# Performance work log

Hardware: AMD Instinct MI355X
Metric: run time of the kernel (lower is better)

## Reference

```python
import jax, jax.numpy as jnp
import numpy as np

B, L, R, F = 16, 64, 256, 64
LIG_NIN, REC_NIN, EIN, EEMB = 32, 40, 16, 16
DEG = 8
E_LIG, E_REC = B * L * DEG, B * R * DEG
NL = 3
PNAMES = ["emb_nW", "emb_nb", "emb_eW", "emb_eb", "hidW", "hidb", "ln0_g", "ln0_b",
          "efW", "efb", "convb", "outW", "outb", "lng", "lnb"]
INT_NAMES = ("lig_src", "lig_dst", "rec_src", "rec_dst")


def _lrelu(v):
    return jax.nn.leaky_relu(v, 0.01)


def _ln(x, g, b):
    m = x.mean(-1, keepdims=True)
    v = ((x - m) ** 2).mean(-1, keepdims=True)
    return (x - m) / jnp.sqrt(v + 1e-5) * g + b


def _side(node_x, edge_x, src, dst, n_nodes, p):
    # GraphEmbedding: linear node/edge embedding
    eh = edge_x @ p["emb_eW"] + p["emb_eb"]                      # [E, EEMB]
    h = _lrelu(node_x @ p["emb_nW"] + p["emb_nb"]) @ p["hidW"] + p["hidb"]
    h = _ln(h, p["ln0_g"], p["ln0_b"])                           # [N, F]
    deg = jax.ops.segment_sum(jnp.ones(src.shape[0], jnp.float32), dst, num_segments=n_nodes)
    deg = jnp.maximum(deg, 1.0)[:, None]
    prev = []
    for i in range(NL):
        hh = _lrelu(h)
        # NNConv: per-edge F x F weight conditioned on edge features
        We = (eh @ p["efW"][i] + p["efb"][i]).reshape(-1, F, F)  # [E, F, F]
        msg = jnp.einsum('ei,eio->eo', hh[src], We)              # [E, F]
        agg = jax.ops.segment_sum(msg, dst, num_segments=n_nodes) / deg + p["convb"][i]
        h = _ln(_lrelu(agg) @ p["outW"][i] + p["outb"][i], p["lng"][i], p["lnb"][i])
        if i >= 2:  # residual to layer i-2
            h = h + prev[i - 2]
        prev.append(h)
    return h


def _forward(fl, lig_src, lig_dst, rec_src, rec_dst):
    lig_p = {n: fl["lig_" + n] for n in PNAMES}
    rec_p = {n: fl["rec_" + n] for n in PNAMES}
    lig_h = _side(fl["lig_x"], fl["lig_e"], lig_src, lig_dst, B * L, lig_p)
    rec_h = _side(fl["rec_x"], fl["rec_e"], rec_src, rec_dst, B * R, rec_p)
    # per-graph einsum('lf,rf->lr') scoring, batched since graphs are equal-sized
    op = jnp.einsum('blf,brf->blr', lig_h.reshape(B, L, F), rec_h.reshape(B, R, F))
    out = op.mean((1, 2))
    return out, op


def setup_inputs() -> dict:
    key = jax.random.key(0)
    it = iter(jax.random.split(key, 80))
    def nrm(shape, s=0.1):
        return jax.random.normal(next(it), shape, jnp.float32) * s
    inp = {}
    inp["lig_x"] = nrm((B * L, LIG_NIN), 1.0)
    inp["rec_x"] = nrm((B * R, REC_NIN), 1.0)
    inp["lig_e"] = nrm((E_LIG, EIN), 1.0)
    inp["rec_e"] = nrm((E_REC, EIN), 1.0)
    def edges(npg, epg, k1, k2):
        offs = (jnp.arange(B) * npg)[:, None]
        s = (jax.random.randint(k1, (B, epg), 0, npg) + offs).reshape(-1).astype(jnp.int32)
        d = (jax.random.randint(k2, (B, epg), 0, npg) + offs).reshape(-1).astype(jnp.int32)
        return s, d
    inp["lig_src"], inp["lig_dst"] = edges(L, L * DEG, next(it), next(it))
    inp["rec_src"], inp["rec_dst"] = edges(R, R * DEG, next(it), next(it))
    for pre, nin in (("lig", LIG_NIN), ("rec", REC_NIN)):
        inp[pre + "_emb_nW"] = nrm((nin, F)); inp[pre + "_emb_nb"] = nrm((F,))
        inp[pre + "_emb_eW"] = nrm((EIN, EEMB)); inp[pre + "_emb_eb"] = nrm((EEMB,))
        inp[pre + "_hidW"] = nrm((F, F)); inp[pre + "_hidb"] = nrm((F,))
        inp[pre + "_ln0_g"] = jnp.ones((F,)); inp[pre + "_ln0_b"] = jnp.zeros((F,))
        inp[pre + "_efW"] = nrm((NL, EEMB, F * F), 0.05); inp[pre + "_efb"] = nrm((NL, F * F), 0.05)
        inp[pre + "_convb"] = nrm((NL, F))
        inp[pre + "_outW"] = nrm((NL, F, F)); inp[pre + "_outb"] = nrm((NL, F))
        inp[pre + "_lng"] = jnp.ones((NL, F)); inp[pre + "_lnb"] = jnp.zeros((NL, F))
    return inp


def reference(lig_x, rec_x, lig_e, rec_e, lig_src, lig_dst, rec_src, rec_dst,
              lig_emb_nW, lig_emb_nb, lig_emb_eW, lig_emb_eb, lig_hidW, lig_hidb,
              lig_ln0_g, lig_ln0_b, lig_efW, lig_efb, lig_convb, lig_outW, lig_outb,
              lig_lng, lig_lnb,
              rec_emb_nW, rec_emb_nb, rec_emb_eW, rec_emb_eb, rec_hidW, rec_hidb,
              rec_ln0_g, rec_ln0_b, rec_efW, rec_efb, rec_convb, rec_outW, rec_outb,
              rec_lng, rec_lnb):
    all_args = dict(locals())
    fl = {k: v for k, v in all_args.items() if k not in INT_NAMES}
    return _forward(fl, lig_src, lig_dst, rec_src, rec_dst)
```

## Files before the change

### kernel.cpp

```cpp
#include <hip/hip_runtime.h>
#include <hip/hip_bf16.h>

#define NLIG 1024
#define NREC 4096
#define NTOT 5120
#define ELIG 8192
#define ETOT 40960
#define TPAD 1092

typedef __bf16 bf16x8 __attribute__((ext_vector_type(8)));
typedef float f32x4 __attribute__((ext_vector_type(4)));

struct Params {
  const float *lig_x, *rec_x, *lig_e, *rec_e;
  const int *lig_src, *lig_dst, *rec_src, *rec_dst;
  const float *nW[2], *nb[2], *eW[2], *eb[2], *hW[2], *hb[2], *g0[2], *b0[2];
  const float *efW[2], *efb[2], *convb[2], *outW[2], *outb[2], *lng[2], *lnb[2];
  float *aggA, *aggB, *prev0, *eh;
  __bf16 *Abf, *Wp;
  int *deg;
  float *out;
};

__device__ __forceinline__ float lrelu(float v){ return v > 0.f ? v : 0.01f * v; }

__device__ __forceinline__ float wsum(float v){
  #pragma unroll
  for (int off = 32; off > 0; off >>= 1) v += __shfl_xor(v, off, 64);
  return v;
}

__global__ __launch_bounds__(256) void k_pre(Params p){
  __shared__ float sW[2][256], sb[2][16], sx[4][40], st[4][64];
  const int tid = threadIdx.x, bid = blockIdx.x;
  const int lane = tid & 63, wid = tid >> 6;
  const int gtid = bid*256 + tid, gwave = bid*4 + wid;

  sW[0][tid] = p.eW[0][tid];
  sW[1][tid] = p.eW[1][tid];
  if (tid < 16){ sb[0][tid] = p.eb[0][tid]; sb[1][tid] = p.eb[1][tid]; }
  __syncthreads();

  if (gtid < 52224){
    int l  = gtid & 63;
    int t2 = gtid >> 6;
    int kk = t2 & 1;
    int t3 = t2 >> 1;
    int ct = t3 % 68;
    int sl = t3 / 68;
    int side = sl / 3, layer = sl % 3;
    int ocol = ct*16 + (l & 15);
    int kslot = ocol >> 6, oo = ocol & 63;
    const float* src = (kslot < 16)
        ? (p.efW[side] + (size_t)layer*16*4096 + (size_t)kslot*4096)
        : (p.efb[side] + (size_t)layer*4096);
    bf16x8 w;
    #pragma unroll
    for (int j = 0; j < 8; j++){
      int i = kk*32 + (l >> 4)*8 + j;
      w[j] = (__bf16)src[i*64 + oo];
    }
    ((bf16x8*)p.Wp)[(size_t)sl*68*2*64 + (ct*2 + kk)*64 + l] = w;
  }

  if (gtid < ETOT){
    int e = gtid;
    int side = e >= ELIG;
    int el = side ? e - ELIG : e;
    const float* ex = (side ? p.rec_e : p.lig_e) + (size_t)el * 16;
    float x[16];
    #pragma unroll
    for (int j = 0; j < 16; j += 4){
      float4 v = *(const float4*)(ex + j);
      x[j] = v.x; x[j+1] = v.y; x[j+2] = v.z; x[j+3] = v.w;
    }
    float s[16];
    #pragma unroll
    for (int k = 0; k < 16; k++){
      float acc = sb[side][k];
      #pragma unroll
      for (int j = 0; j < 16; j++) acc += x[j] * sW[side][j*16 + k];
      s[k] = acc;
    }
    float* ehp = p.eh + (size_t)e * 16;
    #pragma unroll
    for (int k = 0; k < 16; k += 4)
      *(float4*)(ehp + k) = make_float4(s[k], s[k+1], s[k+2], s[k+3]);
  }

  for (int i = gtid; i < NTOT*64; i += 65536){ p.aggA[i] = 0.f; p.aggB[i] = 0.f; }
  if (gtid < 16) p.out[gtid] = 0.f;

  for (int n = gwave; n < NTOT; n += 1024){
    int side = n >= NLIG;
    int nl = side ? n - NLIG : n;
    int nin = side ? 40 : 32;
    const float* x = (side ? p.rec_x : p.lig_x) + (size_t)nl * nin;
    if (lane < nin) sx[wid][lane] = x[lane];
    float tv = p.nb[side][lane];
    const float* nw = p.nW[side];
    for (int j = 0; j < nin; j++) tv += sx[wid][j] * nw[j*64 + lane];
    st[wid][lane] = lrelu(tv);
    float hv = p.hb[side][lane];
    const float* hw = p.hW[side];
    #pragma unroll 8
    for (int j = 0; j < 64; j++) hv += st[wid][j] * hw[j*64 + lane];
    float m = wsum(hv) * (1.f/64.f);
    float d = hv - m;
    float v = wsum(d*d) * (1.f/64.f);
    float o = d * rsqrtf(v + 1e-5f) * p.g0[side][lane] + p.b0[side][lane];
    p.Abf[(size_t)n*64 + lane] = (__bf16)lrelu(o);
  }
}

__global__ __launch_bounds__(1024) void k_layer(Params p, int layer){
  const int tid = threadIdx.x, bid = blockIdx.x;
  const int lane = tid & 63, wid = tid >> 6;
  int side, r0, gr0, ebase, ecnt, egbase;
  const int *srcArr, *dstArr;
  if (bid < 64){
    side = 0; int b = bid >> 2, w = bid & 3;
    r0 = b*64 + w*16; gr0 = r0; ebase = b*512; ecnt = 512; egbase = ebase;
    srcArr = p.lig_src; dstArr = p.lig_dst;
  } else {
    side = 1; int g = bid - 64; int b = g >> 4, w = g & 15;
    r0 = b*256 + w*16; gr0 = NLIG + r0; ebase = b*2048; ecnt = 2048; egbase = ELIG + ebase;
    srcArr = p.rec_src; dstArr = p.rec_dst;
  }
  float* aggR = (layer == 1) ? p.aggA : p.aggB;
  float* aggW = (layer == 1) ? p.aggB : p.aggA;

  __shared__ __bf16 Tl[16][TPAD];
  __shared__ __bf16 albf[16][64];
  __shared__ float sa[16][64];
  __shared__ unsigned int elist[2048];
  __shared__ int scnt[16], sbase[16], scur[16], dcnt[16];

  if (tid < 16){ scnt[tid] = 0; dcnt[tid] = 0; }
  __syncthreads();

  for (int i = tid; i < ecnt; i += 1024){
    int s = srcArr[ebase + i];
    if ((unsigned)(s - r0) < 16u) atomicAdd(&scnt[s - r0], 1);
    if (layer == 0){
      int d = dstArr[ebase + i];
      if ((unsigned)(d - r0) < 16u) atomicAdd(&dcnt[d - r0], 1);
    }
  }
  __syncthreads();
  if (tid < 64){
    int v = (lane < 16) ? scnt[lane] : 0;
    int pre = v;
    #pragma unroll
    for (int off = 1; off < 16; off <<= 1){
      int u = __shfl_up(pre, off, 64);
      if (lane >= off) pre += u;
    }
    if (lane < 16){ sbase[lane] = pre - v; scur[lane] = pre - v; }
  }
  if (layer == 0 && tid < 16) p.deg[gr0 + tid] = dcnt[tid];
  __syncthreads();
  for (int i = tid; i < ecnt; i += 1024){
    int s = srcArr[ebase + i];
    if ((unsigned)(s - r0) < 16u){
      int d = dstArr[ebase + i];
      int pos = atomicAdd(&scur[s - r0], 1);
      elist[pos] = ((unsigned)d << 16) | (unsigned)i;
    }
  }

  if (layer > 0){
    int lm1 = layer - 1;
    int rl = wid;
    int n = gr0 + rl;
    float a = aggR[(size_t)n*64 + lane];
    aggR[(size_t)n*64 + lane] = 0.f;
    float dg = fmaxf((float)p.deg[n], 1.f);
    a = lrelu(a / dg + p.convb[side][lm1*64 + lane]);
    sa[wid][lane] = a;
    float hv = p.outb[side][lm1*64 + lane];
    const float* ow = p.outW[side] + (size_t)lm1*4096;
    #pragma unroll 8
    for (int j = 0; j < 64; j++) hv += sa[wid][j] * ow[j*64 + lane];
    float m = wsum(hv) * (1.f/64.f);
    float d = hv - m;
    float v = wsum(d*d) * (1.f/64.f);
    float o = d * rsqrtf(v + 1e-5f) * p.lng[side][lm1*64 + lane] + p.lnb[side][lm1*64 + lane];
    if (layer == 1) p.prev0[(size_t)n*64 + lane] = o;
    albf[rl][lane] = (__bf16)lrelu(o);
  }
  __syncthreads();

  bf16x8 a0, a1;
  if (layer == 0){
    const bf16x8* A = (const bf16x8*)(p.Abf + (size_t)(gr0 + (lane & 15))*64 + (lane >> 4)*8);
    a0 = A[0]; a1 = A[4];
  } else {
    #pragma unroll
    for (int j = 0; j < 8; j++){
      a0[j] = albf[lane & 15][(lane >> 4)*8 + j];
      a1[j] = albf[lane & 15][32 + (lane >> 4)*8 + j];
    }
  }
  const bf16x8* Wb = (const bf16x8*)p.Wp + (size_t)(side*3 + layer)*68*2*64;
  int orow = (lane >> 4)*4, ocol = lane & 15;
  for (int ct = wid; ct < 68; ct += 16){
    bf16x8 b0 = Wb[(ct*2 + 0)*64 + lane];
    bf16x8 b1 = Wb[(ct*2 + 1)*64 + lane];
    f32x4 d = {0.f, 0.f, 0.f, 0.f};
    d = __builtin_amdgcn_mfma_f32_16x16x32_bf16(a0, b0, d, 0, 0, 0);
    d = __builtin_amdgcn_mfma_f32_16x16x32_bf16(a1, b1, d, 0, 0, 0);
    int col = ct*16 + ocol;
    Tl[orow+0][col] = (__bf16)d[0];
    Tl[orow+1][col] = (__bf16)d[1];
    Tl[orow+2][col] = (__bf16)d[2];
    Tl[orow+3][col] = (__bf16)d[3];
  }
  __syncthreads();

  {
    int s = wid;
    int cnt = scnt[s];
    if (cnt > 0){
      float t[17];
      #pragma unroll
      for (int k = 0; k < 17; k++) t[k] = (float)Tl[s][k*64 + lane];
      int base = sbase[s];
      auto doe = [&](int idx){
        unsigned v = elist[base + idx];
        int gd = (int)(v >> 16) + (side ? NLIG : 0);
        int leid = (int)(v & 0xffffu);
        const float4* ehp = (const float4*)(p.eh + (size_t)(egbase + leid)*16);
        float4 v0 = ehp[0], v1 = ehp[1], v2 = ehp[2], v3 = ehp[3];
        float m = t[16];
        m += v0.x*t[0]  + v0.y*t[1]  + v0.z*t[2]  + v0.w*t[3];
        m += v1.x*t[4]  + v1.y*t[5]  + v1.z*t[6]  + v1.w*t[7];
        m += v2.x*t[8]  + v2.y*t[9]  + v2.z*t[10] + v2.w*t[11];
        m += v3.x*t[12] + v3.y*t[13] + v3.z*t[14] + v3.w*t[15];
        atomicAdd(&aggW[(size_t)gd*64 + lane], m);
      };
      int i = 0;
      for (; i + 2 <= cnt; i += 2){ doe(i); doe(i+1); }
      if (i < cnt) doe(i);
    }
  }
}

__global__ __launch_bounds__(1024) void k_final(Params p){
  const int tid = threadIdx.x, bid = blockIdx.x;
  const int lane = tid & 63, wid = tid >> 6;
  int b = bid >> 4, rt = bid & 15;
  __shared__ float slh[64][65];
  __shared__ float srh[16][65];
  __shared__ float owl[2][4096];
  __shared__ float sa[16][64];
  __shared__ float ps[16];

  for (int idx = tid; idx < 4096; idx += 1024){
    owl[0][idx] = p.outW[0][2*4096 + idx];
    owl[1][idx] = p.outW[1][2*4096 + idx];
  }
  __syncthreads();

  for (int rr = wid; rr < 80; rr += 16){
    int side = rr >= 64;
    int n = side ? (NLIG + b*256 + rt*16 + (rr - 64)) : (b*64 + rr);
    float a = p.aggA[(size_t)n*64 + lane];
    float dg = fmaxf((float)p.deg[n], 1.f);
    a = lrelu(a / dg + p.convb[side][128 + lane]);
    sa[wid][lane] = a;
    float hv = p.outb[side][128 + lane];
    const float* ow = &owl[side][0];
    #pragma unroll 8
    for (int j = 0; j < 64; j++) hv += sa[wid][j] * ow[j*64 + lane];
    float m = wsum(hv) * (1.f/64.f);
    float d = hv - m;
    float v = wsum(d*d) * (1.f/64.f);
    float o = d * rsqrtf(v + 1e-5f) * p.lng[side][128 + lane] + p.lnb[side][128 + lane];
    o += p.prev0[(size_t)n*64 + lane];
    if (side) srh[rr - 64][lane] = o; else slh[rr][lane] = o;
  }
  __syncthreads();

  int r = tid & 15, lg = tid >> 4;
  float acc = 0.f;
  #pragma unroll 8
  for (int f = 0; f < 64; f++) acc += slh[lg][f] * srh[r][f];
  p.out[16 + (size_t)b*16384 + (size_t)lg*256 + rt*16 + r] = acc;

  float psum = wsum(acc);
  if (lane == 0) ps[wid] = psum;
  __syncthreads();
  if (tid == 0){
    float s = 0.f;
    #pragma unroll
    for (int i = 0; i < 16; i++) s += ps[i];
    atomicAdd(&p.out[b], s * (1.f/16384.f));
  }
}

extern "C" void kernel_launch(void* const* d_in, const int* in_sizes, int n_in,
                              void* d_out, int out_size, void* d_ws, size_t ws_size,
                              hipStream_t stream){
  Params p;
  p.lig_x  = (const float*)d_in[0];
  p.rec_x  = (const float*)d_in[1];
  p.lig_e  = (const float*)d_in[2];
  p.rec_e  = (const float*)d_in[3];
  p.lig_src = (const int*)d_in[4];
  p.lig_dst = (const int*)d_in[5];
  p.rec_src = (const int*)d_in[6];
  p.rec_dst = (const int*)d_in[7];
  for (int s = 0; s < 2; s++){
    const int o = 8 + s*15;
    p.nW[s]   = (const float*)d_in[o+0];  p.nb[s]   = (const float*)d_in[o+1];
    p.eW[s]   = (const float*)d_in[o+2];  p.eb[s]   = (const float*)d_in[o+3];
    p.hW[s]   = (const float*)d_in[o+4];  p.hb[s]   = (const float*)d_in[o+5];
    p.g0[s]   = (const float*)d_in[o+6];  p.b0[s]   = (const float*)d_in[o+7];
    p.efW[s]  = (const float*)d_in[o+8];  p.efb[s]  = (const float*)d_in[o+9];
    p.convb[s]= (const float*)d_in[o+10]; p.outW[s] = (const float*)d_in[o+11];
    p.outb[s] = (const float*)d_in[o+12]; p.lng[s]  = (const float*)d_in[o+13];
    p.lnb[s]  = (const float*)d_in[o+14];
  }
  char* W = (char*)d_ws;
  p.aggA  = (float*)W;  W += (size_t)NTOT*64*4;
  p.aggB  = (float*)W;  W += (size_t)NTOT*64*4;
  p.prev0 = (float*)W;  W += (size_t)NTOT*64*4;
  p.eh    = (float*)W;  W += (size_t)ETOT*16*4;
  p.Abf   = (__bf16*)W; W += (size_t)NTOT*64*2;
  p.Wp    = (__bf16*)W; W += (size_t)2*3*68*2*64*8*2;
  p.deg   = (int*)W;    W += (size_t)NTOT*4;
  p.out   = (float*)d_out;

  k_pre<<<256, 256, 0, stream>>>(p);
  k_layer<<<320, 1024, 0, stream>>>(p, 0);
  k_layer<<<320, 1024, 0, stream>>>(p, 1);
  k_layer<<<320, 1024, 0, stream>>>(p, 2);
  k_final<<<256, 1024, 0, stream>>>(p);
}
```

Before: 116.3 us.

## Build edge buckets once in pre-kernel and reuse across all layers

Moves the per-block edge bucketing (counting by source row, prefix scan, scatter into an edge list) out of each of the three layer launches and into the pre-kernel, which now runs on 320 blocks and writes the buckets, bases and counts to global workspace. Each layer kernel then reads its bucket list from global memory with a coalesced per-wave load and broadcasts entries by shuffle, instead of rebuilding the list in shared memory every launch. This removes repeated scans of the src/dst arrays, the shared atomics and two barriers per layer, and frees the 8 KB shared edge list. The cost is extra global traffic for the bucket arrays and more work in the pre-kernel. The layer kernel also gains a min-blocks hint in its launch bounds.

```diff
diff --git a/kernel.cpp b/kernel.cpp
--- a/kernel.cpp
+++ b/kernel.cpp
@@ -19,6 +19,8 @@
   float *aggA, *aggB, *prev0, *eh;
   __bf16 *Abf, *Wp;
   int *deg;
+  unsigned *bkt;
+  int *bktbase, *bktcnt;
   float *out;
 };
 
@@ -30,8 +32,24 @@
   return v;
 }
 
+__device__ __forceinline__ void window(int bid, int& side, int& r0, int& gr0,
+                                       int& ebase, int& ecnt, int& egbase,
+                                       const int*& srcArr, const int*& dstArr,
+                                       const Params& p){
+  if (bid < 64){
+    side = 0; int b = bid >> 2, w = bid & 3;
+    r0 = b*64 + w*16; gr0 = r0; ebase = b*512; ecnt = 512; egbase = ebase;
+    srcArr = p.lig_src; dstArr = p.lig_dst;
+  } else {
+    side = 1; int g = bid - 64; int b = g >> 4, w = g & 15;
+    r0 = b*256 + w*16; gr0 = NLIG + r0; ebase = b*2048; ecnt = 2048; egbase = ELIG + ebase;
+    srcArr = p.rec_src; dstArr = p.rec_dst;
+  }
+}
+
 __global__ __launch_bounds__(256) void k_pre(Params p){
   __shared__ float sW[2][256], sb[2][16], sx[4][40], st[4][64];
+  __shared__ int scnt[16], sbase[16], scur[16], dcnt[16];
   const int tid = threadIdx.x, bid = blockIdx.x;
   const int lane = tid & 63, wid = tid >> 6;
   const int gtid = bid*256 + tid, gwave = bid*4 + wid;
@@ -39,6 +57,7 @@
   sW[0][tid] = p.eW[0][tid];
   sW[1][tid] = p.eW[1][tid];
   if (tid < 16){ sb[0][tid] = p.eb[0][tid]; sb[1][tid] = p.eb[1][tid]; }
+  if (tid < 16){ scnt[tid] = 0; dcnt[tid] = 0; }
   __syncthreads();
 
   if (gtid < 52224){
@@ -88,10 +107,10 @@
       *(float4*)(ehp + k) = make_float4(s[k], s[k+1], s[k+2], s[k+3]);
   }
 
-  for (int i = gtid; i < NTOT*64; i += 65536){ p.aggA[i] = 0.f; p.aggB[i] = 0.f; }
+  for (int i = gtid; i < NTOT*64; i += 320*256){ p.aggA[i] = 0.f; p.aggB[i] = 0.f; }
   if (gtid < 16) p.out[gtid] = 0.f;
 
-  for (int n = gwave; n < NTOT; n += 1024){
+  for (int n = gwave; n < NTOT; n += 1280){
     int side = n >= NLIG;
     int nl = side ? n - NLIG : n;
     int nin = side ? 40 : 32;
@@ -111,68 +130,57 @@
     float o = d * rsqrtf(v + 1e-5f) * p.g0[side][lane] + p.b0[side][lane];
     p.Abf[(size_t)n*64 + lane] = (__bf16)lrelu(o);
   }
-}
-
-__global__ __launch_bounds__(1024) void k_layer(Params p, int layer){
+
+  int side, r0, gr0, ebase, ecnt, egbase;
+  const int *srcArr, *dstArr;
+  window(bid, side, r0, gr0, ebase, ecnt, egbase, srcArr, dstArr, p);
+
+  for (int i = tid; i < ecnt; i += 256){
+    int s = srcArr[ebase + i];
+    if ((unsigned)(s - r0) < 16u) atomicAdd(&scnt[s - r0], 1);
+    int d = dstArr[ebase + i];
+    if ((unsigned)(d - r0) < 16u) atomicAdd(&dcnt[d - r0], 1);
+  }
+  __syncthreads();
+  if (tid < 64){
+    int v = (lane < 16) ? scnt[lane] : 0;
+    int pre = v;
+    #pragma unroll
+    for (int off = 1; off < 16; off <<= 1){
+      int u = __shfl_up(pre, off, 64);
+      if (lane >= off) pre += u;
+    }
+    if (lane < 16){ sbase[lane] = pre - v; scur[lane] = pre - v; }
+  }
+  if (tid < 16) p.deg[gr0 + tid] = dcnt[tid];
+  __syncthreads();
+  for (int i = tid; i < ecnt; i += 256){
+    int s = srcArr[ebase + i];
+    if ((unsigned)(s - r0) < 16u){
+      int d = dstArr[ebase + i];
+      int pos = atomicAdd(&scur[s - r0], 1);
+      p.bkt[(size_t)bid*2048 + pos] = ((unsigned)d << 16) | (unsigned)i;
+    }
+  }
+  if (tid < 16){ p.bktbase[bid*16 + tid] = sbase[tid]; p.bktcnt[bid*16 + tid] = scnt[tid]; }
+}
+
+__global__ __launch_bounds__(1024, 8) void k_layer(Params p, int layer){
   const int tid = threadIdx.x, bid = blockIdx.x;
   const int lane = tid & 63, wid = tid >> 6;
   int side, r0, gr0, ebase, ecnt, egbase;
   const int *srcArr, *dstArr;
-  if (bid < 64){
-    side = 0; int b = bid >> 2, w = bid & 3;
-    r0 = b*64 + w*16; gr0 = r0; ebase = b*512; ecnt = 512; egbase = ebase;
-    srcArr = p.lig_src; dstArr = p.lig_dst;
-  } else {
-    side = 1; int g = bid - 64; int b = g >> 4, w = g & 15;
-    r0 = b*256 + w*16; gr0 = NLIG + r0; ebase = b*2048; ecnt = 2048; egbase = ELIG + ebase;
-    srcArr = p.rec_src; dstArr = p.rec_dst;
-  }
+  window(bid, side, r0, gr0, ebase, ecnt, egbase, srcArr, dstArr, p);
   float* aggR = (layer == 1) ? p.aggA : p.aggB;
   float* aggW = (layer == 1) ? p.aggB : p.aggA;
 
   __shared__ __bf16 Tl[16][TPAD];
   __shared__ __bf16 albf[16][64];
   __shared__ float sa[16][64];
-  __shared__ unsigned int elist[2048];
-  __shared__ int scnt[16], sbase[16], scur[16], dcnt[16];
-
-  if (tid < 16){ scnt[tid] = 0; dcnt[tid] = 0; }
-  __syncthreads();
-
-  for (int i = tid; i < ecnt; i += 1024){
-    int s = srcArr[ebase + i];
-    if ((unsigned)(s - r0) < 16u) atomicAdd(&scnt[s - r0], 1);
-    if (layer == 0){
-      int d = dstArr[ebase + i];
-      if ((unsigned)(d - r0) < 16u) atomicAdd(&dcnt[d - r0], 1);
-    }
-  }
-  __syncthreads();
-  if (tid < 64){
-    int v = (lane < 16) ? scnt[lane] : 0;
-    int pre = v;
-    #pragma unroll
-    for (int off = 1; off < 16; off <<= 1){
-      int u = __shfl_up(pre, off, 64);
-      if (lane >= off) pre += u;
-    }
-    if (lane < 16){ sbase[lane] = pre - v; scur[lane] = pre - v; }
-  }
-  if (layer == 0 && tid < 16) p.deg[gr0 + tid] = dcnt[tid];
-  __syncthreads();
-  for (int i = tid; i < ecnt; i += 1024){
-    int s = srcArr[ebase + i];
-    if ((unsigned)(s - r0) < 16u){
-      int d = dstArr[ebase + i];
-      int pos = atomicAdd(&scur[s - r0], 1);
-      elist[pos] = ((unsigned)d << 16) | (unsigned)i;
-    }
-  }
 
   if (layer > 0){
     int lm1 = layer - 1;
-    int rl = wid;
-    int n = gr0 + rl;
+    int n = gr0 + wid;
     float a = aggR[(size_t)n*64 + lane];
     aggR[(size_t)n*64 + lane] = 0.f;
     float dg = fmaxf((float)p.deg[n], 1.f);
@@ -187,7 +195,7 @@
     float v = wsum(d*d) * (1.f/64.f);
     float o = d * rsqrtf(v + 1e-5f) * p.lng[side][lm1*64 + lane] + p.lnb[side][lm1*64 + lane];
     if (layer == 1) p.prev0[(size_t)n*64 + lane] = o;
-    albf[rl][lane] = (__bf16)lrelu(o);
+    albf[wid][lane] = (__bf16)lrelu(o);
   }
   __syncthreads();
 
@@ -219,29 +227,34 @@
   __syncthreads();
 
   {
-    int s = wid;
-    int cnt = scnt[s];
+    int cnt  = p.bktcnt[bid*16 + wid];
     if (cnt > 0){
       float t[17];
       #pragma unroll
-      for (int k = 0; k < 17; k++) t[k] = (float)Tl[s][k*64 + lane];
-      int base = sbase[s];
-      auto doe = [&](int idx){
-        unsigned v = elist[base + idx];
-        int gd = (int)(v >> 16) + (side ? NLIG : 0);
-        int leid = (int)(v & 0xffffu);
-        const float4* ehp = (const float4*)(p.eh + (size_t)(egbase + leid)*16);
-        float4 v0 = ehp[0], v1 = ehp[1], v2 = ehp[2], v3 = ehp[3];
-        float m = t[16];
-        m += v0.x*t[0]  + v0.y*t[1]  + v0.z*t[2]  + v0.w*t[3];
-        m += v1.x*t[4]  + v1.y*t[5]  + v1.z*t[6]  + v1.w*t[7];
-        m += v2.x*t[8]  + v2.y*t[9]  + v2.z*t[10] + v2.w*t[11];
-        m += v3.x*t[12] + v3.y*t[13] + v3.z*t[14] + v3.w*t[15];
-        atomicAdd(&aggW[(size_t)gd*64 + lane], m);
-      };
-      int i = 0;
-      for (; i + 2 <= cnt; i += 2){ doe(i); doe(i+1); }
-      if (i < cnt) doe(i);
+      for (int k = 0; k < 17; k++) t[k] = (float)Tl[wid][k*64 + lane];
+      size_t base = (size_t)bid*2048 + p.bktbase[bid*16 + wid];
+      for (int c0 = 0; c0 < cnt; c0 += 64){
+        int nn = min(64, cnt - c0);
+        unsigned ew = (lane < nn) ? p.bkt[base + c0 + lane] : 0u;
+        auto doe = [&](unsigned v){
+          int gd = (int)(v >> 16) + (side ? NLIG : 0);
+          int leid = (int)(v & 0xffffu);
+          const float4* ehp = (const float4*)(p.eh + (size_t)(egbase + leid)*16);
+          float4 v0 = ehp[0], v1 = ehp[1], v2 = ehp[2], v3 = ehp[3];
+          float m = t[16];
+          m += v0.x*t[0]  + v0.y*t[1]  + v0.z*t[2]  + v0.w*t[3];
+          m += v1.x*t[4]  + v1.y*t[5]  + v1.z*t[6]  + v1.w*t[7];
+          m += v2.x*t[8]  + v2.y*t[9]  + v2.z*t[10] + v2.w*t[11];
+          m += v3.x*t[12] + v3.y*t[13] + v3.z*t[14] + v3.w*t[15];
+          atomicAdd(&aggW[(size_t)gd*64 + lane], m);
+        };
+        int j = 0;
+        for (; j + 2 <= nn; j += 2){
+          unsigned e0 = __shfl(ew, j, 64), e1 = __shfl(ew, j+1, 64);
+          doe(e0); doe(e1);
+        }
+        if (j < nn) doe(__shfl(ew, j, 64));
+      }
     }
   }
 }
@@ -330,9 +343,12 @@
   p.Abf   = (__bf16*)W; W += (size_t)NTOT*64*2;
   p.Wp    = (__bf16*)W; W += (size_t)2*3*68*2*64*8*2;
   p.deg   = (int*)W;    W += (size_t)NTOT*4;
+  p.bkt   = (unsigned*)W; W += (size_t)320*2048*4;
+  p.bktbase = (int*)W;  W += (size_t)320*16*4;
+  p.bktcnt  = (int*)W;  W += (size_t)320*16*4;
   p.out   = (float*)d_out;
 
-  k_pre<<<256, 256, 0, stream>>>(p);
+  k_pre<<<320, 256, 0, stream>>>(p);
   k_layer<<<320, 1024, 0, stream>>>(p, 0);
   k_layer<<<320, 1024, 0, stream>>>(p, 1);
   k_layer<<<320, 1024, 0, stream>>>(p, 2);
```

Measured after the change: 119.9 us. 3.2% more time.
